# Optimization experiments

Measured on AMD Instinct MI355X. Metric: run time of the kernel, lower is better.

Reference implementation:

```python
import jax, jax.numpy as jnp
import numpy as np

B, T, C, H = 2, 2048, 1024, 16
D = C // H  # head dim = 64

def setup_inputs() -> dict:
    key = jax.random.key(0)
    k1, k2 = jax.random.split(key)
    x = jax.random.normal(k1, (B, T, C), dtype=jnp.float32)
    W_attn = jax.random.normal(k2, (3 * C, C), dtype=jnp.float32) * 0.02
    return {"x": x, "W_attn": W_attn}

def reference(x, W_attn):
    Bx, Tx, Cx = x.shape
    qkv = jnp.einsum('btc,fc->btf', x, W_attn)  # fused QKV projection (bias=False)
    q, k, v = jnp.split(qkv, 3, axis=-1)
    # [B, H, T, D]
    q = q.reshape(Bx, Tx, H, D).transpose(0, 2, 1, 3)
    k = k.reshape(Bx, Tx, H, D).transpose(0, 2, 1, 3)
    v = v.reshape(Bx, Tx, H, D).transpose(0, 2, 1, 3)
    scale = 1.0 / jnp.sqrt(jnp.asarray(D, dtype=q.dtype))
    scores = jnp.einsum('bhqd,bhkd->bhqk', q, k) * scale  # [B,H,T,T]
    causal = jnp.tril(jnp.ones((Tx, Tx), dtype=bool))
    scores = jnp.where(causal[None, None], scores, jnp.asarray(-jnp.inf, dtype=scores.dtype))
    attn = jax.nn.softmax(scores, axis=-1)
    y = jnp.einsum('bhqk,bhkd->bhqd', attn, v)
    y = y.transpose(0, 2, 1, 3).reshape(Bx, Tx, Cx)  # merge heads; dropout=0 at eval
    return y
```

## Files before the change

kernel.cpp:

```cpp
#include <hip/hip_runtime.h>
#include <hip/hip_bf16.h>

#define Bn 2
#define Tn 2048
#define Cn 1024
#define Hn 16
#define Dn 64
#define Mdim 4096
#define Ndim 3072
#define Kdim 1024

typedef unsigned short u16;
typedef __attribute__((ext_vector_type(8))) short bf16x8;
typedef __attribute__((ext_vector_type(4))) float f32x4;

__device__ __forceinline__ u16 f2bf(float v) {
    unsigned int x = __builtin_bit_cast(unsigned int, v);
    unsigned int r = (x + 0x7fffu + ((x >> 16) & 1u)) >> 16;
    return (u16)r;
}

__device__ __forceinline__ unsigned int pack2(float a, float b) {
    return (unsigned int)f2bf(a) | ((unsigned int)f2bf(b) << 16);
}

__device__ __forceinline__ unsigned int cvt_pk_bf16(float lo, float hi) {
    unsigned int r;
    asm("v_cvt_pk_bf16_f32 %0, %1, %2" : "=v"(r) : "v"(lo), "v"(hi));
    return r;
}

__device__ __forceinline__ void async16(const void* g, void* l) {
    __builtin_amdgcn_global_load_lds(
        (const __attribute__((address_space(1))) void*)g,
        (__attribute__((address_space(3))) void*)(unsigned int)(unsigned long long)l,
        16, 0, 0);
}

__device__ __forceinline__ int probe_inline(const unsigned int* __restrict__ X, int tid) {
    const int lane = tid & 63;
    int cnt = 0;
    #pragma unroll
    for (int i = 0; i < 8; i++) {
        unsigned int e = (X[lane * 8 + i] >> 7) & 0xFFu;
        cnt += (e >= 100u && e < 134u) ? 1 : 0;
    }
    #pragma unroll
    for (int off = 1; off < 64; off <<= 1) cnt += __shfl_xor(cnt, off);
    return cnt > 256 ? 1 : 0;
}

#define NXC ((size_t)Mdim * Kdim / 8)
#define NWC ((size_t)Ndim * Kdim / 8)

__global__ __launch_bounds__(256) void convert_in(
        const void* __restrict__ Xv, const void* __restrict__ Wv,
        u16* __restrict__ Xb, u16* __restrict__ Wb, int* __restrict__ flag) {
    const int isbf = probe_inline((const unsigned int*)Xv, threadIdx.x);
    if (blockIdx.x == 0 && threadIdx.x == 0) *flag = isbf;
    size_t i = (size_t)blockIdx.x * 256 + threadIdx.x;
    if (i >= NXC + NWC) return;
    const void* src; u16* dst; size_t off;
    if (i < NXC) { src = Xv; dst = Xb; off = i; }
    else         { src = Wv; dst = Wb; off = i - NXC; }
    if (isbf) {
        ((uint4*)dst)[off] = ((const uint4*)src)[off];
    } else {
        const float4* s = (const float4*)src + off * 2;
        float4 a = s[0], b = s[1];
        ((uint4*)dst)[off] = (uint4){pack2(a.x, a.y), pack2(a.z, a.w),
                                     pack2(b.x, b.y), pack2(b.z, b.w)};
    }
}

__global__ __launch_bounds__(256) void qkv_gemm(
        const u16* __restrict__ Xb, const u16* __restrict__ Wb,
        u16* __restrict__ Q, u16* __restrict__ Kc, u16* __restrict__ Vt) {
    __shared__ __align__(16) u16 sA[128 * 32];
    __shared__ __align__(16) u16 sB[128 * 32];

    const int tid  = threadIdx.x;
    const int lane = tid & 63;
    const int wv   = tid >> 6;
    const int quad = lane >> 4;
    const int r16  = lane & 15;
    const int m0 = blockIdx.y * 128;
    const int n0 = blockIdx.x * 128;
    const int wm = (wv >> 1) * 64;
    const int wn = (wv & 1) * 64;
    const int l4 = lane >> 2;
    const int c8 = (lane & 3) * 8;

    f32x4 acc[4][4];
    #pragma unroll
    for (int i = 0; i < 4; i++)
        #pragma unroll
        for (int j = 0; j < 4; j++)
            acc[i][j] = (f32x4){0.f, 0.f, 0.f, 0.f};

    for (int k0 = 0; k0 < Kdim; k0 += 32) {
        __syncthreads();
        #pragma unroll
        for (int i = 0; i < 2; i++) {
            const int rg = (wv + 4 * i) * 16;
            async16(Xb + (size_t)(m0 + rg + l4) * Kdim + k0 + c8, sA + rg * 32);
            async16(Wb + (size_t)(n0 + rg + l4) * Kdim + k0 + c8, sB + rg * 32);
        }
        __syncthreads();

        bf16x8 af[4], bfr[4];
        #pragma unroll
        for (int mt = 0; mt < 4; mt++)
            af[mt] = *(const bf16x8*)(sA + (wm + mt * 16 + r16) * 32 + quad * 8);
        #pragma unroll
        for (int nt = 0; nt < 4; nt++)
            bfr[nt] = *(const bf16x8*)(sB + (wn + nt * 16 + r16) * 32 + quad * 8);
        #pragma unroll
        for (int mt = 0; mt < 4; mt++)
            #pragma unroll
            for (int nt = 0; nt < 4; nt++)
                acc[mt][nt] = __builtin_amdgcn_mfma_f32_16x16x32_bf16(
                    af[mt], bfr[nt], acc[mt][nt], 0, 0, 0);
    }

    #pragma unroll
    for (int mt = 0; mt < 4; mt++) {
        #pragma unroll
        for (int nt = 0; nt < 4; nt++) {
            #pragma unroll
            for (int r = 0; r < 4; r++) {
                int m = m0 + wm + mt * 16 + quad * 4 + r;
                int f = n0 + wn + nt * 16 + r16;
                float v = acc[mt][nt][r];
                int b = m >> 11, t = m & 2047;
                int sect = f >> 10;
                int h = (f >> 6) & 15;
                int d = f & 63;
                int bh = b * Hn + h;
                if (sect == 0) {
                    Q[((size_t)(bh * Tn + t)) * Dn + d] = f2bf(v * 0.125f);
                } else if (sect == 1) {
                    Kc[((size_t)(bh * Tn + t)) * Dn + d] = f2bf(v);
                } else {
                    Vt[((size_t)(bh * Dn + d)) * Tn + t] = f2bf(v);
                }
            }
        }
    }
}


#define SWZ(R, C) ((R) * 64 + (((C) * 8) ^ (((R) & 7) << 3)))

#define STAGE(KB, BUF) do {                                                    \
    const int kbase_ = (KB) * 64;                                              \
    if (w < 2) {                                                               \
        _Pragma("unroll")                                                      \
        for (int i = 0; i < 4; i++) {                                          \
            const int seg = w * 4 + i;             \
            async16(Kc + qkBase + (size_t)(kbase_ + seg * 8 + rl) * Dn + gc8,  \
                    &sK[BUF][seg * 512]);                                      \
        }                                                                      \
    } else {                                                                   \
        _Pragma("unroll")                                                      \
        for (int i = 0; i < 4; i++) {                                          \
            const int seg = (w - 2) * 4 + i;     \
            async16(Vt + vBase + (size_t)(seg * 8 + rl) * Tn + kbase_ + gc8,   \
                    &sV[BUF][seg * 512]);                                      \
        }                                                                      \
    }                                                                          \
} while (0)

#define COMPUTE(KB, BUF) do {                                                  \
    const int kbase_ = (KB) * 64;                                              \
    const bool diag_ = ((KB) == nkb_w - 1);                                    \
    bf16x8 kf[4][2], vf[4][2];                                                 \
    _Pragma("unroll")                                                          \
    for (int nt = 0; nt < 4; nt++) {                                           \
        kf[nt][0] = *(const bf16x8*)&sK[BUF][SWZ(nt * 16 + r16, quad)];        \
        kf[nt][1] = *(const bf16x8*)&sK[BUF][SWZ(nt * 16 + r16, 4 + quad)];    \
    }                                                                          \
    _Pragma("unroll")                                                          \
    for (int dt = 0; dt < 4; dt++) {                                           \
        vf[dt][0] = *(const bf16x8*)&sV[BUF][SWZ(dt * 16 + r16, quad)];        \
        vf[dt][1] = *(const bf16x8*)&sV[BUF][SWZ(dt * 16 + r16, 4 + quad)];    \
    }                                                                          \
    _Pragma("unroll")                                                          \
    for (int mt = 0; mt < 2; mt++) {                                           \
        f32x4 s[4];                                                            \
        __builtin_amdgcn_s_setprio(1);                                         \
        _Pragma("unroll")                                                      \
        for (int nt = 0; nt < 4; nt++) {                                       \
            f32x4 z = (f32x4){-8.f, -8.f, -8.f, -8.f};                         \
            z = __builtin_amdgcn_mfma_f32_16x16x32_bf16(kf[nt][0], aq[mt][0], z, 0, 0, 0); \
            z = __builtin_amdgcn_mfma_f32_16x16x32_bf16(kf[nt][1], aq[mt][1], z, 0, 0, 0); \
            s[nt] = z;                                                         \
        }                                                                      \
        __builtin_amdgcn_s_setprio(0);                                         \
        if (diag_) {                                                           \
            const int query = qw0 + mt * 16 + r16;                             \
            _Pragma("unroll")                                                  \
            for (int nt = 0; nt < 4; nt++)                                     \
                _Pragma("unroll")                                              \
                for (int r = 0; r < 4; r++) {                                  \
                    int key = kbase_ + nt * 16 + quad * 4 + r;                 \
                    if (key > query) s[nt][r] = -1e30f;                        \
                }                                                              \
        }                                                                      \
        unsigned int pk[4][2];                                                 \
        _Pragma("unroll")                                                      \
        for (int nt = 0; nt < 4; nt++) {                                       \
            float p0 = __expf(s[nt][0]);                                       \
            float p1 = __expf(s[nt][1]);                                       \
            float p2 = __expf(s[nt][2]);                                       \
            float p3 = __expf(s[nt][3]);                                       \
            lacc[mt] += (p0 + p1) + (p2 + p3);                                 \
            pk[nt][0] = cvt_pk_bf16(p0, p1);                                   \
            pk[nt][1] = cvt_pk_bf16(p2, p3);                                   \
        }                                                                      \
        _Pragma("unroll")                                                      \
        for (int kc = 0; kc < 2; kc++) {                                       \
            int4 bq;                                                           \
            _Pragma("unroll")                                                  \
            for (int h = 0; h < 2; h++) {                                      \
                unsigned int a = pk[kc * 2 + 0][h];                            \
                unsigned int b = pk[kc * 2 + 1][h];                            \
                auto t = __builtin_amdgcn_permlane32_swap(a, b, false, false); \
                auto u = __builtin_amdgcn_permlane16_swap(t[0], t[1], false, false); \
                ((unsigned int*)&bq)[0 + h] = u[0];                            \
                ((unsigned int*)&bq)[2 + h] = u[1];                            \
            }                                                                  \
            bf16x8 bqv = __builtin_bit_cast(bf16x8, bq);                       \
            __builtin_amdgcn_s_setprio(1);                                     \
            _Pragma("unroll")                                                  \
            for (int dt = 0; dt < 4; dt++)                                     \
                o[mt][dt] = __builtin_amdgcn_mfma_f32_16x16x32_bf16(           \
                    vf[dt][kc], bqv, o[mt][dt], 0, 0, 0);                      \
            __builtin_amdgcn_s_setprio(0);                                     \
        }                                                                      \
    }                                                                          \
} while (0)

__global__ __launch_bounds__(256) void attn(
        const u16* __restrict__ Q, const u16* __restrict__ Kc,
        const u16* __restrict__ Vt, void* __restrict__ Y,
        const int* __restrict__ flag) {
    __shared__ __align__(16) u16 sK[2][4096];
    __shared__ __align__(16) u16 sV[2][4096];

    const int isbf = *flag;
    const int tid  = threadIdx.x;
    const int lane = tid & 63;
    const int w    = tid >> 6;
    const int quad = lane >> 4;
    const int r16  = lane & 15;
    const int bid  = blockIdx.x;
    const int bh   = bid & (Bn * Hn - 1);
    const int j    = bid >> 5;
    const int qt   = (j < 8) ? (15 - j) : (j - 8);
    const int q0   = qt * 128;
    const int qw0  = q0 + w * 32;
    const size_t qkBase = (size_t)bh * Tn * Dn;
    const size_t vBase  = (size_t)bh * Dn * Tn;

    const int rl  = lane >> 3;
    const int gc8 = (((lane & 7) ^ rl)) * 8;

    bf16x8 aq[2][2];
    #pragma unroll
    for (int mt = 0; mt < 2; mt++) {
        const u16* qp = Q + qkBase + (size_t)(qw0 + mt * 16 + r16) * Dn;
        aq[mt][0] = *(const bf16x8*)(qp + quad * 8);
        aq[mt][1] = *(const bf16x8*)(qp + 32 + quad * 8);
    }

    float lacc[2] = {0.f, 0.f};
    f32x4 o[2][4];
    #pragma unroll
    for (int mt = 0; mt < 2; mt++)
        #pragma unroll
        for (int dt = 0; dt < 4; dt++) o[mt][dt] = (f32x4){0.f, 0.f, 0.f, 0.f};

    const int kbmax = 2 * qt + 1;
    const int nkb_w = 2 * qt + 1 + (w >> 1);

    STAGE(0, 0);
    __syncthreads();

    for (int kb = 0; kb <= kbmax; kb++) {
        const int cur = kb & 1;
        if (kb < kbmax) STAGE(kb + 1, cur ^ 1);
        if (kb < nkb_w) COMPUTE(kb, cur);
        __syncthreads();
    }

    const int b = bh >> 4, h = bh & 15;
    #pragma unroll
    for (int mt = 0; mt < 2; mt++) {
        float den = lacc[mt];
        den += __shfl_xor(den, 16);
        den += __shfl_xor(den, 32);
        float rden = 1.f / fmaxf(den, 1e-30f);
        int t = qw0 + mt * 16 + r16;
        #pragma unroll
        for (int dt = 0; dt < 4; dt++) {
            float v0 = o[mt][dt][0] * rden;
            float v1 = o[mt][dt][1] * rden;
            float v2 = o[mt][dt][2] * rden;
            float v3 = o[mt][dt][3] * rden;
            int c = h * Dn + dt * 16 + quad * 4;
            size_t idx = ((size_t)(b * Tn + t)) * Cn + c;
            if (isbf) {
                ushort4 pk4 = {f2bf(v0), f2bf(v1), f2bf(v2), f2bf(v3)};
                *(ushort4*)((u16*)Y + idx) = pk4;
            } else {
                float4 f4 = {v0, v1, v2, v3};
                *(float4*)((float*)Y + idx) = f4;
            }
        }
    }
}

extern "C" void kernel_launch(void* const* d_in, const int* in_sizes, int n_in,
                              void* d_out, int out_size, void* d_ws, size_t ws_size,
                              hipStream_t stream) {
    const void* X = d_in[0];
    const void* W = d_in[1];
    void* Y = d_out;

    const size_t per = (size_t)Bn * Hn * Tn * Dn;
    int* flag = (int*)d_ws;
    u16* Q  = (u16*)((char*)d_ws + 256);
    u16* Kc = Q + per;
    u16* Vt = Kc + per;
    u16* Xb = Vt + per;
    u16* Wb = Xb + (size_t)Mdim * Kdim;

    {
        const size_t nch = NXC + NWC;
        convert_in<<<dim3((unsigned)((nch + 255) / 256)), 256, 0, stream>>>(X, W, Xb, Wb, flag);
    }
    qkv_gemm<<<dim3(Ndim / 128, Mdim / 128), 256, 0, stream>>>(Xb, Wb, Q, Kc, Vt);
    attn<<<dim3(Bn * Hn * (Tn / 128)), 256, 0, stream>>>(Q, Kc, Vt, Y, flag);
}
```

Before: 154.7 us.

## Rewrite QKV GEMM with 256x256 tiles, double-buffered async loads, and XOR-swizzled LDS

```diff
diff --git a/kernel.cpp b/kernel.cpp
--- a/kernel.cpp
+++ b/kernel.cpp
@@ -73,78 +73,137 @@
     }
 }
 
-__global__ __launch_bounds__(256) void qkv_gemm(
+#define NTq (Kdim / 64)
+
+#define PBAR() do { asm volatile("" ::: "memory"); \
+                    __builtin_amdgcn_s_barrier();  \
+                    asm volatile("" ::: "memory"); } while (0)
+#define VMW(n) asm volatile("s_waitcnt vmcnt(" #n ")" ::: "memory")
+
+#define QSTAGE_A(QIDX, BUF, KOFF) \
+    async16(Xb + (size_t)(m0 + (QIDX) * 64 + srow) * Kdim + (KOFF) + gc, \
+            &sA[BUF][(QIDX) * 4096 + w * 512])
+#define QSTAGE_B(QIDX, BUF, KOFF) \
+    async16(Wb + (size_t)(n0 + (QIDX) * 64 + srow) * Kdim + (KOFF) + gc, \
+            &sB[BUF][(QIDX) * 4096 + w * 512])
+
+#define RDA(MQ, BUF) do {                                                  \
+    _Pragma("unroll")                                                      \
+    for (int mt = 0; mt < 4; mt++) {                                       \
+        const u16* p = &sA[BUF][(wm + (MQ) * 64 + mt * 16 + r16) * 64];    \
+        af[mt][0] = *(const bf16x8*)(p + cx0);                             \
+        af[mt][1] = *(const bf16x8*)(p + (cx0 ^ 32));                      \
+    } } while (0)
+
+#define RDB(NQ, BUF) do {                                                  \
+    _Pragma("unroll")                                                      \
+    for (int nt = 0; nt < 2; nt++) {                                       \
+        const u16* p = &sB[BUF][(wn + (NQ) * 32 + nt * 16 + r16) * 64];    \
+        bf[NQ][nt][0] = *(const bf16x8*)(p + cx0);                         \
+        bf[NQ][nt][1] = *(const bf16x8*)(p + (cx0 ^ 32));                  \
+    } } while (0)
+
+#define MM(MQ, NQ) do {                                                    \
+    __builtin_amdgcn_s_setprio(1);                                         \
+    _Pragma("unroll")                                                      \
+    for (int mt = 0; mt < 4; mt++)                                         \
+        _Pragma("unroll")                                                  \
+        for (int nt = 0; nt < 2; nt++) {                                   \
+            acc[(MQ)*4+mt][(NQ)*2+nt] = __builtin_amdgcn_mfma_f32_16x16x32_bf16( \
+                af[mt][0], bf[NQ][nt][0], acc[(MQ)*4+mt][(NQ)*2+nt], 0,0,0);     \
+            acc[(MQ)*4+mt][(NQ)*2+nt] = __builtin_amdgcn_mfma_f32_16x16x32_bf16( \
+                af[mt][1], bf[NQ][nt][1], acc[(MQ)*4+mt][(NQ)*2+nt], 0,0,0);     \
+        }                                                                  \
+    __builtin_amdgcn_s_setprio(0);                                         \
+} while (0)
+
+__global__ __launch_bounds__(512, 2) void qkv_gemm(
         const u16* __restrict__ Xb, const u16* __restrict__ Wb,
         u16* __restrict__ Q, u16* __restrict__ Kc, u16* __restrict__ Vt) {
-    __shared__ __align__(16) u16 sA[128 * 32];
-    __shared__ __align__(16) u16 sB[128 * 32];
+    __shared__ __align__(16) u16 sA[2][256 * 64];
+    __shared__ __align__(16) u16 sB[2][256 * 64];
 
     const int tid  = threadIdx.x;
     const int lane = tid & 63;
-    const int wv   = tid >> 6;
+    const int w    = tid >> 6;
     const int quad = lane >> 4;
     const int r16  = lane & 15;
-    const int m0 = blockIdx.y * 128;
-    const int n0 = blockIdx.x * 128;
-    const int wm = (wv >> 1) * 64;
-    const int wn = (wv & 1) * 64;
-    const int l4 = lane >> 2;
-    const int c8 = (lane & 3) * 8;
-
-    f32x4 acc[4][4];
-    #pragma unroll
-    for (int i = 0; i < 4; i++)
+    const int wm   = (w >> 2) * 128;
+    const int wn   = (w & 3) * 64;
+
+    const int l0 = blockIdx.x;
+    const int nl = (l0 & 7) * 24 + (l0 >> 3);
+    const int m0 = (nl / 12) * 256;
+    const int n0 = (nl % 12) * 256;
+
+    const int lr   = lane >> 3;
+    const int gc   = ((lane & 7) ^ lr) * 8;
+    const int srow = w * 8 + lr;
+
+    const int cx0 = (quad ^ (r16 & 7)) * 8;
+
+    f32x4 acc[8][4];
+    #pragma unroll
+    for (int i = 0; i < 8; i++)
         #pragma unroll
         for (int j = 0; j < 4; j++)
             acc[i][j] = (f32x4){0.f, 0.f, 0.f, 0.f};
 
-    for (int k0 = 0; k0 < Kdim; k0 += 32) {
-        __syncthreads();
-        #pragma unroll
-        for (int i = 0; i < 2; i++) {
-            const int rg = (wv + 4 * i) * 16;
-            async16(Xb + (size_t)(m0 + rg + l4) * Kdim + k0 + c8, sA + rg * 32);
-            async16(Wb + (size_t)(n0 + rg + l4) * Kdim + k0 + c8, sB + rg * 32);
-        }
-        __syncthreads();
-
-        bf16x8 af[4], bfr[4];
-        #pragma unroll
-        for (int mt = 0; mt < 4; mt++)
-            af[mt] = *(const bf16x8*)(sA + (wm + mt * 16 + r16) * 32 + quad * 8);
-        #pragma unroll
-        for (int nt = 0; nt < 4; nt++)
-            bfr[nt] = *(const bf16x8*)(sB + (wn + nt * 16 + r16) * 32 + quad * 8);
-        #pragma unroll
-        for (int mt = 0; mt < 4; mt++)
+    bf16x8 af[4][2];
+    bf16x8 bf[2][2][2];
+
+    #pragma unroll
+    for (int q = 0; q < 4; q++) { QSTAGE_A(q, 0, 0); QSTAGE_B(q, 0, 0); }
+    VMW(0);
+    PBAR();
+
+    int koff = 0;
+    for (int kt = 0; kt < NTq; kt++) {
+        const int cur = kt & 1, nxt = cur ^ 1;
+        const bool pf = (kt + 1 < NTq);
+        const int kn = koff + 64;
+        RDA(0, cur); RDB(0, cur);
+        if (pf) { QSTAGE_B(0, nxt, kn); QSTAGE_B(1, nxt, kn); }
+        PBAR(); MM(0, 0); PBAR();
+        RDB(1, cur);
+        if (pf) { QSTAGE_B(2, nxt, kn); QSTAGE_B(3, nxt, kn); }
+        VMW(4); PBAR(); MM(0, 1); PBAR();
+        RDA(1, cur);
+        if (pf) { QSTAGE_A(0, nxt, kn); QSTAGE_A(2, nxt, kn); }
+        PBAR(); MM(1, 1); PBAR();
+        if (pf) { QSTAGE_A(1, nxt, kn); QSTAGE_A(3, nxt, kn); }
+        VMW(2); PBAR(); MM(1, 0); PBAR();
+        koff = kn;
+    }
+
+    const int sect = n0 >> 10;
+    #pragma unroll
+    for (int mq = 0; mq < 2; mq++)
+    #pragma unroll
+    for (int mt = 0; mt < 4; mt++)
+    #pragma unroll
+    for (int nq = 0; nq < 2; nq++)
+    #pragma unroll
+    for (int nt = 0; nt < 2; nt++) {
+        f32x4 v4 = acc[mq * 4 + mt][nq * 2 + nt];
+        const int mBase = m0 + wm + mq * 64 + mt * 16 + quad * 4;
+        const int f = n0 + wn + nq * 32 + nt * 16 + r16;
+        const int b = mBase >> 11;
+        const int t0 = mBase & 2047;
+        const int h = (f >> 6) & 15;
+        const int d = f & 63;
+        const int bh = b * Hn + h;
+        if (sect == 0) {
             #pragma unroll
-            for (int nt = 0; nt < 4; nt++)
-                acc[mt][nt] = __builtin_amdgcn_mfma_f32_16x16x32_bf16(
-                    af[mt], bfr[nt], acc[mt][nt], 0, 0, 0);
-    }
-
-    #pragma unroll
-    for (int mt = 0; mt < 4; mt++) {
-        #pragma unroll
-        for (int nt = 0; nt < 4; nt++) {
+            for (int r = 0; r < 4; r++)
+                Q[((size_t)(bh * Tn + t0 + r)) * Dn + d] = f2bf(v4[r] * 0.125f);
+        } else if (sect == 1) {
             #pragma unroll
-            for (int r = 0; r < 4; r++) {
-                int m = m0 + wm + mt * 16 + quad * 4 + r;
-                int f = n0 + wn + nt * 16 + r16;
-                float v = acc[mt][nt][r];
-                int b = m >> 11, t = m & 2047;
-                int sect = f >> 10;
-                int h = (f >> 6) & 15;
-                int d = f & 63;
-                int bh = b * Hn + h;
-                if (sect == 0) {
-                    Q[((size_t)(bh * Tn + t)) * Dn + d] = f2bf(v * 0.125f);
-                } else if (sect == 1) {
-                    Kc[((size_t)(bh * Tn + t)) * Dn + d] = f2bf(v);
-                } else {
-                    Vt[((size_t)(bh * Dn + d)) * Tn + t] = f2bf(v);
-                }
-            }
+            for (int r = 0; r < 4; r++)
+                Kc[((size_t)(bh * Tn + t0 + r)) * Dn + d] = f2bf(v4[r]);
+        } else {
+            ushort4 pk4 = {f2bf(v4[0]), f2bf(v4[1]), f2bf(v4[2]), f2bf(v4[3])};
+            *(ushort4*)(Vt + ((size_t)(bh * Dn + d)) * Tn + t0) = pk4;
         }
     }
 }
@@ -340,6 +399,6 @@
         const size_t nch = NXC + NWC;
         convert_in<<<dim3((unsigned)((nch + 255) / 256)), 256, 0, stream>>>(X, W, Xb, Wb, flag);
     }
-    qkv_gemm<<<dim3(Ndim / 128, Mdim / 128), 256, 0, stream>>>(Xb, Wb, Q, Kc, Vt);
+    qkv_gemm<<<dim3((Mdim / 256) * (Ndim / 256)), 512, 0, stream>>>(Xb, Wb, Q, Kc, Vt);
     attn<<<dim3(Bn * Hn * (Tn / 128)), 256, 0, stream>>>(Q, Kc, Vt, Y, flag);
 }
```

Result: faster. 148.2 us (-4.2%).
